# Performance work log

Hardware: AMD Instinct MI355X
Metric: run time of the kernel (lower is better)

## Reference

```python
import jax, jax.numpy as jnp
import numpy as np

EPS = 1e-8  # matches torch F.cosine_similarity eps


def setup_inputs() -> dict:
    key = jax.random.key(0)
    k1, k2, k3 = jax.random.split(key, 3)
    S, B, H = 16, 512, 2048
    OGLogits = jax.random.normal(k1, (B, H), dtype=jnp.float32)
    enhancedSamplesLogits = jax.random.normal(k2, (S, B, H), dtype=jnp.float32)
    W = jax.random.normal(k3, (H, H), dtype=jnp.float32) * (1.0 / np.sqrt(H))
    b = jnp.zeros((H,), dtype=jnp.float32)
    return {"OGLogits": OGLogits, "enhancedSamplesLogits": enhancedSamplesLogits, "W": W, "b": b}


def reference(OGLogits, enhancedSamplesLogits, W, b):
    # Original torch code builds the full (S*B, B) cosine-similarity matrix and
    # keeps only the diagonal via an eye mask; mathematically that equals the
    # per-pair cosine similarity cos(enhanced[s,b], OG[b]), computed directly here.
    e_norm = jnp.linalg.norm(enhancedSamplesLogits, axis=-1)          # (S, B)
    o_norm = jnp.linalg.norm(OGLogits, axis=-1)                       # (B,)
    dots = jnp.einsum('sbh,bh->sb', enhancedSamplesLogits, OGLogits)  # (S, B)
    sims = dots / jnp.maximum(e_norm * o_norm[None, :], EPS)          # (S, B)
    weighted = enhancedSamplesLogits * sims[..., None]                # (S, B, H)
    weightedRep = weighted.mean(axis=0)                               # (B, H)
    return weightedRep @ W.T + b                                      # (B, H)
```

## Files before the change

kernel.cpp:

```cpp
#include <hip/hip_runtime.h>

#define S_DIM 16
#define B_DIM 512
#define H_DIM 2048
#define EPS 1e-8f

typedef short bf16x8 __attribute__((ext_vector_type(8)));
typedef float f32x16 __attribute__((ext_vector_type(16)));

__device__ __forceinline__ unsigned short f2bf(float f) {
    union { float f; unsigned int u; } v; v.f = f;
    unsigned int u = v.u;
    unsigned int r = (u + 0x7fffu + ((u >> 16) & 1u)) >> 16;
    return (unsigned short)r;
}

__device__ __forceinline__ float dot4(const float4& a, const float4& b) {
    return a.x*b.x + a.y*b.y + a.z*b.z + a.w*b.w;
}

__global__ __launch_bounds__(512, 4) void fused_kernel(
    const float* __restrict__ OG, const float* __restrict__ E,
    const float* __restrict__ W, unsigned short* __restrict__ wrep,
    unsigned short* __restrict__ Wb) {
    const int b = blockIdx.x;
    const int t = threadIdx.x;
    const int lane = t & 63;
    const int wave = t >> 6;

    __shared__ float4 buf[8][512];
    __shared__ float4 ogs[512];
    __shared__ float red[8];

    const float4* w4 = (const float4*)W;
    ushort4* wb4 = (ushort4*)Wb;
    const size_t wbase = (size_t)b * 2048 + t;

    float4 wv0 = w4[wbase];
    float4 wv1 = w4[wbase + 512];
    const float4* og4 = (const float4*)(OG + (size_t)b * H_DIM);
    float4 o = og4[t];

    const float4* e4a = (const float4*)(E + ((size_t)wave * B_DIM + b) * H_DIM);
    const float4* e4b = (const float4*)(E + ((size_t)(wave + 8) * B_DIM + b) * H_DIM);
    float4 ea[8], eb[8];
    #pragma unroll
    for (int i = 0; i < 8; ++i) {
        ea[i] = e4a[i * 64 + lane];
        eb[i] = e4b[i * 64 + lane];
    }
    float4 wv2 = w4[wbase + 1024];
    float4 wv3 = w4[wbase + 1536];

    ogs[t] = o;
    float p = dot4(o, o);
    #pragma unroll
    for (int m = 32; m >= 1; m >>= 1) p += __shfl_xor(p, m, 64);
    if (lane == 0) red[wave] = p;

    {
        ushort4 c0, c1;
        c0.x = f2bf(wv0.x); c0.y = f2bf(wv0.y); c0.z = f2bf(wv0.z); c0.w = f2bf(wv0.w);
        c1.x = f2bf(wv1.x); c1.y = f2bf(wv1.y); c1.z = f2bf(wv1.z); c1.w = f2bf(wv1.w);
        wb4[wbase] = c0;
        wb4[wbase + 512] = c1;
    }
    __syncthreads();

    float og2 = 0.f;
    #pragma unroll
    for (int w = 0; w < 8; ++w) og2 += red[w];
    const float onorm = sqrtf(og2);

    float da = 0.f, na = 0.f, db = 0.f, nb = 0.f;
    #pragma unroll
    for (int i = 0; i < 8; ++i) {
        float4 g = ogs[i * 64 + lane];
        da += dot4(ea[i], g); na += dot4(ea[i], ea[i]);
        db += dot4(eb[i], g); nb += dot4(eb[i], eb[i]);
    }
    #pragma unroll
    for (int m = 32; m >= 1; m >>= 1) {
        da += __shfl_xor(da, m, 64);
        na += __shfl_xor(na, m, 64);
        db += __shfl_xor(db, m, 64);
        nb += __shfl_xor(nb, m, 64);
    }
    const float sima = da / fmaxf(sqrtf(na) * onorm, EPS);
    const float simb = db / fmaxf(sqrtf(nb) * onorm, EPS);

    #pragma unroll
    for (int i = 0; i < 8; ++i) {
        float4 v;
        v.x = ea[i].x * sima + eb[i].x * simb;
        v.y = ea[i].y * sima + eb[i].y * simb;
        v.z = ea[i].z * sima + eb[i].z * simb;
        v.w = ea[i].w * sima + eb[i].w * simb;
        buf[wave][i * 64 + lane] = v;
    }
    {
        ushort4 c2, c3;
        c2.x = f2bf(wv2.x); c2.y = f2bf(wv2.y); c2.z = f2bf(wv2.z); c2.w = f2bf(wv2.w);
        c3.x = f2bf(wv3.x); c3.y = f2bf(wv3.y); c3.z = f2bf(wv3.z); c3.w = f2bf(wv3.w);
        wb4[wbase + 1024] = c2;
        wb4[wbase + 1536] = c3;
    }
    __syncthreads();

    float4 s = buf[0][t];
    #pragma unroll
    for (int w = 1; w < 8; ++w) {
        float4 v = buf[w][t];
        s.x += v.x; s.y += v.y; s.z += v.z; s.w += v.w;
    }
    const float sc = 1.f / (float)S_DIM;
    ushort4 ob;
    ob.x = f2bf(s.x * sc); ob.y = f2bf(s.y * sc);
    ob.z = f2bf(s.z * sc); ob.w = f2bf(s.w * sc);
    ((ushort4*)wrep)[(size_t)b * (H_DIM / 4) + t] = ob;
}

__global__ __launch_bounds__(256) void gemm_kernel(
    const unsigned short* __restrict__ A, const unsigned short* __restrict__ Wb,
    const float* __restrict__ bias, float* __restrict__ out) {
    const int bid = blockIdx.x;
    const int xcd = bid & 7, j = bid >> 3;
    const int n0 = (xcd * 4 + (j & 3)) * 64;
    const int m0 = (j >> 2) * 64;

    __shared__ unsigned short As[2][64 * 64];
    __shared__ unsigned short Bs[2][64 * 64];

    const int t = threadIdx.x;
    const int lane = t & 63;
    const int wave = t >> 6;
    const int wm = (wave & 1) * 32;
    const int wn = (wave >> 1) * 32;

    const int lr = t >> 2, lq = t & 3;
    const unsigned short* ap = A  + (size_t)(m0 + lr) * H_DIM + lq * 16;
    const unsigned short* bp = Wb + (size_t)(n0 + lr) * H_DIM + lq * 16;

    const int swz = (lr & 7) << 4;
    const int w0 = lr * 64 + (((lq * 32) ^ swz) >> 1);
    const int w1 = lr * 64 + (((lq * 32 + 16) ^ swz) >> 1);

    f32x16 acc0 = {0.f,0.f,0.f,0.f,0.f,0.f,0.f,0.f,
                   0.f,0.f,0.f,0.f,0.f,0.f,0.f,0.f};
    f32x16 acc1 = acc0;

    const int row = lane & 31;
    const int hi = lane >> 5;
    const int rswz = (row & 7) << 4;
    int roffA[4], roffB[4];
    #pragma unroll
    for (int ks = 0; ks < 4; ++ks) {
        const int x = ((ks * 32 + hi * 16) ^ rswz) >> 1;
        roffA[ks] = (wm + row) * 64 + x;
        roffB[ks] = (wn + row) * 64 + x;
    }

    uint4 ra0 = *(const uint4*)(ap);
    uint4 ra1 = *(const uint4*)(ap + 8);
    uint4 rb0 = *(const uint4*)(bp);
    uint4 rb1 = *(const uint4*)(bp + 8);
    uint4 sa0 = *(const uint4*)(ap + 64);
    uint4 sa1 = *(const uint4*)(ap + 72);
    uint4 sb0 = *(const uint4*)(bp + 64);
    uint4 sb1 = *(const uint4*)(bp + 72);
    *(uint4*)&As[0][w0] = ra0;
    *(uint4*)&As[0][w1] = ra1;
    *(uint4*)&Bs[0][w0] = rb0;
    *(uint4*)&Bs[0][w1] = rb1;
    __syncthreads();

    #define MFMA_TILE(BUF)                                                        \
    {                                                                             \
        _Pragma("unroll")                                                         \
        for (int ks = 0; ks < 2; ++ks) {                                          \
            bf16x8 afA = *(const bf16x8*)&As[BUF][roffA[ks]];                     \
            bf16x8 bfA = *(const bf16x8*)&Bs[BUF][roffB[ks]];                     \
            acc0 = __builtin_amdgcn_mfma_f32_32x32x16_bf16(afA, bfA, acc0, 0,0,0);\
            bf16x8 afB = *(const bf16x8*)&As[BUF][roffA[ks + 2]];                 \
            bf16x8 bfB = *(const bf16x8*)&Bs[BUF][roffB[ks + 2]];                 \
            acc1 = __builtin_amdgcn_mfma_f32_32x32x16_bf16(afB, bfB, acc1, 0,0,0);\
        }                                                                         \
    }

    for (int ki = 0; ki < 32; ki += 2) {
        if (ki + 2 < 32) {
            ra0 = *(const uint4*)(ap + (ki + 2) * 64);
            ra1 = *(const uint4*)(ap + (ki + 2) * 64 + 8);
            rb0 = *(const uint4*)(bp + (ki + 2) * 64);
            rb1 = *(const uint4*)(bp + (ki + 2) * 64 + 8);
        }
        MFMA_TILE(0);
        *(uint4*)&As[1][w0] = sa0;
        *(uint4*)&As[1][w1] = sa1;
        *(uint4*)&Bs[1][w0] = sb0;
        *(uint4*)&Bs[1][w1] = sb1;
        __syncthreads();
        if (ki + 3 < 32) {
            sa0 = *(const uint4*)(ap + (ki + 3) * 64);
            sa1 = *(const uint4*)(ap + (ki + 3) * 64 + 8);
            sb0 = *(const uint4*)(bp + (ki + 3) * 64);
            sb1 = *(const uint4*)(bp + (ki + 3) * 64 + 8);
        }
        MFMA_TILE(1);
        if (ki + 2 < 32) {
            *(uint4*)&As[0][w0] = ra0;
            *(uint4*)&As[0][w1] = ra1;
            *(uint4*)&Bs[0][w0] = rb0;
            *(uint4*)&Bs[0][w1] = rb1;
            __syncthreads();
        }
    }
    #undef MFMA_TILE

    const int col = lane & 31;
    const float bias0 = bias[n0 + wn + col];
    #pragma unroll
    for (int r = 0; r < 16; ++r) {
        const int mr = (r & 3) + 8 * (r >> 2) + 4 * hi;
        out[(size_t)(m0 + wm + mr) * H_DIM + n0 + wn + col] = acc0[r] + acc1[r] + bias0;
    }
}

extern "C" void kernel_launch(void* const* d_in, const int* in_sizes, int n_in,
                              void* d_out, int out_size, void* d_ws, size_t ws_size,
                              hipStream_t stream) {
    const float* OG   = (const float*)d_in[0];
    const float* E    = (const float*)d_in[1];
    const float* W    = (const float*)d_in[2];
    const float* bias = (const float*)d_in[3];
    float* out = (float*)d_out;

    unsigned short* wrep = (unsigned short*)d_ws;
    unsigned short* Wb   = wrep + (size_t)B_DIM * H_DIM;

    fused_kernel<<<B_DIM, 512, 0, stream>>>(OG, E, W, wrep, Wb);
    gemm_kernel<<<256, 256, 0, stream>>>(wrep, Wb, bias, out);
}
```

Baseline: 120.7 us.

## Split GEMM K-slices across waves with 2x2 register tiles and LDS reduction

The GEMM kernel previously gave each wave its own 32x32 output quadrant and had it walk the full K of every 64-wide tile. Now each wave takes one 16-wide K slice and computes the whole 64x64 tile as four 32x32 MFMA accumulators. Each A and B fragment is then loaded once from LDS and reused twice, cutting LDS reads per MFMA. In exchange, a 64KB shared buffer and an extra barrier are needed to sum the four partial tiles at the end, and the larger LDS footprint lowers occupancy.

```diff
diff --git a/kernel.cpp b/kernel.cpp
--- a/kernel.cpp
+++ b/kernel.cpp
@@ -130,12 +130,11 @@
 
     __shared__ unsigned short As[2][64 * 64];
     __shared__ unsigned short Bs[2][64 * 64];
+    __shared__ float red[4][16][256];
 
     const int t = threadIdx.x;
     const int lane = t & 63;
-    const int wave = t >> 6;
-    const int wm = (wave & 1) * 32;
-    const int wn = (wave >> 1) * 32;
+    const int kh = t >> 6;
 
     const int lr = t >> 2, lq = t & 3;
     const unsigned short* ap = A  + (size_t)(m0 + lr) * H_DIM + lq * 16;
@@ -147,18 +146,11 @@
 
     f32x16 acc0 = {0.f,0.f,0.f,0.f,0.f,0.f,0.f,0.f,
                    0.f,0.f,0.f,0.f,0.f,0.f,0.f,0.f};
-    f32x16 acc1 = acc0;
+    f32x16 acc1 = acc0, acc2 = acc0, acc3 = acc0;
 
     const int row = lane & 31;
     const int hi = lane >> 5;
-    const int rswz = (row & 7) << 4;
-    int roffA[4], roffB[4];
-    #pragma unroll
-    for (int ks = 0; ks < 4; ++ks) {
-        const int x = ((ks * 32 + hi * 16) ^ rswz) >> 1;
-        roffA[ks] = (wm + row) * 64 + x;
-        roffB[ks] = (wn + row) * 64 + x;
-    }
+    const int off0 = row * 64 + (((kh * 32 + hi * 16) ^ ((row & 7) << 4)) >> 1);
 
     uint4 ra0 = *(const uint4*)(ap);
     uint4 ra1 = *(const uint4*)(ap + 8);
@@ -176,15 +168,14 @@
 
     #define MFMA_TILE(BUF)                                                        \
     {                                                                             \
-        _Pragma("unroll")                                                         \
-        for (int ks = 0; ks < 2; ++ks) {                                          \
-            bf16x8 afA = *(const bf16x8*)&As[BUF][roffA[ks]];                     \
-            bf16x8 bfA = *(const bf16x8*)&Bs[BUF][roffB[ks]];                     \
-            acc0 = __builtin_amdgcn_mfma_f32_32x32x16_bf16(afA, bfA, acc0, 0,0,0);\
-            bf16x8 afB = *(const bf16x8*)&As[BUF][roffA[ks + 2]];                 \
-            bf16x8 bfB = *(const bf16x8*)&Bs[BUF][roffB[ks + 2]];                 \
-            acc1 = __builtin_amdgcn_mfma_f32_32x32x16_bf16(afB, bfB, acc1, 0,0,0);\
-        }                                                                         \
+        bf16x8 a0 = *(const bf16x8*)&As[BUF][off0];                               \
+        bf16x8 a1 = *(const bf16x8*)&As[BUF][off0 + 2048];                        \
+        bf16x8 b0 = *(const bf16x8*)&Bs[BUF][off0];                               \
+        bf16x8 b1 = *(const bf16x8*)&Bs[BUF][off0 + 2048];                        \
+        acc0 = __builtin_amdgcn_mfma_f32_32x32x16_bf16(a0, b0, acc0, 0, 0, 0);    \
+        acc1 = __builtin_amdgcn_mfma_f32_32x32x16_bf16(a0, b1, acc1, 0, 0, 0);    \
+        acc2 = __builtin_amdgcn_mfma_f32_32x32x16_bf16(a1, b0, acc2, 0, 0, 0);    \
+        acc3 = __builtin_amdgcn_mfma_f32_32x32x16_bf16(a1, b1, acc3, 0, 0, 0);    \
     }
 
     for (int ki = 0; ki < 32; ki += 2) {
@@ -217,12 +208,37 @@
     }
     #undef MFMA_TILE
 
-    const int col = lane & 31;
-    const float bias0 = bias[n0 + wn + col];
-    #pragma unroll
-    for (int r = 0; r < 16; ++r) {
-        const int mr = (r & 3) + 8 * (r >> 2) + 4 * hi;
-        out[(size_t)(m0 + wm + mr) * H_DIM + n0 + wn + col] = acc0[r] + acc1[r] + bias0;
+    #define DUMP(C, ACC)                                                         \
+        { _Pragma("unroll")                                                      \
+          for (int r4 = 0; r4 < 4; ++r4) {                                       \
+              float4 v = {(ACC)[r4*4], (ACC)[r4*4+1], (ACC)[r4*4+2], (ACC)[r4*4+3]}; \
+              *(float4*)&red[kh][(C)*4 + r4][lane << 2] = v;                     \
+          } }
+    DUMP(0, acc0); DUMP(1, acc1); DUMP(2, acc2); DUMP(3, acc3);
+    #undef DUMP
+    __syncthreads();
+
+    const int qm = kh >> 1, qn = kh & 1;
+    const int col = n0 + qn * 32 + row;
+    const float bias0 = bias[col];
+    #pragma unroll
+    for (int i = 0; i < 4; ++i) {
+        const int s = kh * 4 + i;
+        float4 v0 = *(float4*)&red[0][s][lane << 2];
+        float4 v1 = *(float4*)&red[1][s][lane << 2];
+        float4 v2 = *(float4*)&red[2][s][lane << 2];
+        float4 v3 = *(float4*)&red[3][s][lane << 2];
+        float4 v;
+        v.x = v0.x + v1.x + v2.x + v3.x;
+        v.y = v0.y + v1.y + v2.y + v3.y;
+        v.z = v0.z + v1.z + v2.z + v3.z;
+        v.w = v0.w + v1.w + v2.w + v3.w;
+        const float vv[4] = {v.x, v.y, v.z, v.w};
+        #pragma unroll
+        for (int rr = 0; rr < 4; ++rr) {
+            const int mr = rr + 8 * i + 4 * hi;
+            out[(size_t)(m0 + qm * 32 + mr) * H_DIM + col] = vv[rr] + bias0;
+        }
     }
 }
 
```

New measurement: 120.1 us. No clear change (-0.5%).
